# Kernel tuning notes

Hardware: AMD Instinct MI355X
Metric: run time of the kernel (lower is better)

Reference implementation:

```python
import jax, jax.numpy as jnp
import numpy as np

N = 2048            # matrix dimension (d_model-sized orthogonal factor)
BATCH = 8192        # number of row-vectors multiplied by the matrix exponential
SIGN = 1            # slogdet sign; 1 means no row negation
TRANSPOSE = False
N_FLAT = N * (N - 1) // 2


def setup_inputs() -> dict:
    key = jax.random.key(0)
    k1, k2 = jax.random.split(key)
    X = jax.random.normal(k1, (BATCH, N), dtype=jnp.float32)
    # small scale keeps the 9-term Taylor series well inside its convergence regime
    S_flat = jax.random.normal(k2, (N_FLAT,), dtype=jnp.float32) * 0.01
    return {"X": X, "S_flat": S_flat}


def _weight(S_flat):
    # unfold: scatter strict upper triangle, antisymmetrize
    rows, cols = jnp.triu_indices(N, k=1)
    M = jnp.zeros((N, N), dtype=S_flat.dtype).at[rows, cols].set(S_flat)
    S = M - M.T
    # truncated Taylor series exp(S) = I + S + S^2/2! + ... + S^9/9!
    T = S
    Q = jnp.eye(N, dtype=S.dtype) + S
    for i in range(2, 10):
        T = (T @ S) / i
        Q = Q + T
    if SIGN == -1:
        if TRANSPOSE:
            Q = Q.at[:, 0].multiply(-1.0)
        else:
            Q = Q.at[0].multiply(-1.0)
    return Q


def reference(X, S_flat):
    return X @ _weight(S_flat)
```

## Files before the change

kernel.cpp:

```cpp
#include <hip/hip_runtime.h>
#include <hip/hip_bf16.h>
#include <stdint.h>

#define N_DIM 2048
#define BATCH_SZ 8192

typedef __bf16 bf16;
typedef __bf16 bf16x4 __attribute__((ext_vector_type(4)));
typedef __bf16 bf16x8 __attribute__((ext_vector_type(8)));
typedef float f32x4 __attribute__((ext_vector_type(4)));

__device__ __forceinline__ void gld16(const bf16* g, bf16* l) {
  __builtin_amdgcn_global_load_lds(
      (const __attribute__((address_space(1))) void*)g,
      (__attribute__((address_space(3))) void*)l, 16, 0, 0);
}

__global__ void unfold_kernel(const float* __restrict__ Sflat,
                              bf16* __restrict__ Wb,
                              bf16* __restrict__ Wtb) {
  int idx = blockIdx.x * blockDim.x + threadIdx.x;
  int i = idx >> 11;
  int j = idx & (N_DIM - 1);
  float v = 0.0f;
  if (i < j) {
    int fi = i * (N_DIM - 1) - ((i * (i - 1)) >> 1) + (j - i - 1);
    v = Sflat[fi];
  } else if (i > j) {
    int fi = j * (N_DIM - 1) - ((j * (j - 1)) >> 1) + (i - j - 1);
    v = -Sflat[fi];
  }
  Wb[idx]  = (bf16)(-v);
  Wtb[idx] = (bf16)(v);
}

__global__ void cast_kernel(const float* __restrict__ in, bf16* __restrict__ out) {
  int t = blockIdx.x * blockDim.x + threadIdx.x;
  float4 v = ((const float4*)in)[t];
  bf16x4 o;
  o.x = (bf16)v.x; o.y = (bf16)v.y; o.z = (bf16)v.z; o.w = (bf16)v.w;
  ((bf16x4*)out)[t] = o;
}

template <int MODE>
__global__ __launch_bounds__(256, 2) void gemm_w(
    const bf16* __restrict__ A, const bf16* __restrict__ Bt,
    bf16* __restrict__ O1, bf16* __restrict__ O2,
    const bf16* __restrict__ Wb, int M, int N, int K) {
  __shared__ __align__(16) bf16 As[3 * 2 * 64 * 32];
  __shared__ __align__(16) bf16 Bs[3 * 2 * 128 * 32];

  const int tid  = threadIdx.x;
  const int lane = tid & 63;
  const int wave = tid >> 6;
  const int wr   = wave >> 1;
  const int wc   = wave & 1;
  const int quad = lane >> 4;
  const int l16  = lane & 15;

  const int nwg    = gridDim.x * gridDim.y;
  const int linear = blockIdx.y * gridDim.x + blockIdx.x;
  const int wg = (linear & 7) * (nwg >> 3) + (linear >> 3);
  const int bx = wg & 15;
  const int by = wg >> 4;
  const int m0 = by * 64;
  const int n0 = bx * 128;

  const int srow  = lane >> 2;
  const int sslot = (lane & 3) ^ ((lane >> 3) & 3);
  const bf16* gA  = A  + (size_t)(m0 + wave * 16 + srow) * K + sslot * 8;
  const bf16* gB1 = Bt + (size_t)(n0 + wave * 16 + srow) * K + sslot * 8;
  const bf16* gB2 = gB1 + (size_t)64 * K;
  bf16* lA  = As + wave * 512;
  bf16* lB1 = Bs + wave * 512;
  bf16* lB2 = Bs + wave * 512 + 2048;

  const int NS = K >> 6;

  auto STAGE = [&](int t, int s) {
#pragma unroll
    for (int k = 0; k < 2; ++k) {
      const size_t ko = (size_t)t * 64 + k * 32;
      gld16(gA  + ko, lA  + (s * 2 + k) * 2048);
      gld16(gB1 + ko, lB1 + (s * 2 + k) * 4096);
      gld16(gB2 + ko, lB2 + (s * 2 + k) * 4096);
    }
  };

  STAGE(0, 0);
  STAGE(1, 1);
  asm volatile("s_waitcnt vmcnt(6)" ::: "memory");
  __builtin_amdgcn_sched_barrier(0);
  __builtin_amdgcn_s_barrier();
  __builtin_amdgcn_sched_barrier(0);

  f32x4 acc[2][4] = {};
  const int rswz = (quad ^ ((l16 >> 1) & 3)) * 8;
  const int arow = wr * 32 + l16;
  const int brow = wc * 64 + l16;

  auto body = [&](int t, int s) {
    if (t + 2 < NS) STAGE(t + 2, (s + 2) % 3);
    bf16x8 af[2][2], bfr[2][4];
#pragma unroll
    for (int k = 0; k < 2; ++k) {
      const bf16* ab = As + (s * 2 + k) * 2048;
      const bf16* bb = Bs + (s * 2 + k) * 4096;
#pragma unroll
      for (int mi = 0; mi < 2; ++mi)
        af[k][mi] = *(const bf16x8*)&ab[(arow + mi * 16) * 32 + rswz];
#pragma unroll
      for (int ni = 0; ni < 4; ++ni)
        bfr[k][ni] = *(const bf16x8*)&bb[(brow + ni * 16) * 32 + rswz];
    }
    __builtin_amdgcn_s_setprio(1);
#pragma unroll
    for (int k = 0; k < 2; ++k)
#pragma unroll
      for (int mi = 0; mi < 2; ++mi)
#pragma unroll
        for (int ni = 0; ni < 4; ++ni)
          acc[mi][ni] = __builtin_amdgcn_mfma_f32_16x16x32_bf16(
              af[k][mi], bfr[k][ni], acc[mi][ni], 0, 0, 0);
    __builtin_amdgcn_s_setprio(0);
    if (t < NS - 1) {
      if (t + 2 < NS)
        asm volatile("s_waitcnt vmcnt(6)" ::: "memory");
      else
        asm volatile("s_waitcnt vmcnt(0)" ::: "memory");
      __builtin_amdgcn_sched_barrier(0);
      __builtin_amdgcn_s_barrier();
      __builtin_amdgcn_sched_barrier(0);
    }
  };

  const int NS3 = NS - (NS % 3);
#pragma unroll 1
  for (int t0 = 0; t0 < NS3; t0 += 3) {
    body(t0, 0);
    body(t0 + 1, 1);
    body(t0 + 2, 2);
  }
#pragma unroll
  for (int u = 0; u < 3; ++u) {
    const int t = NS3 + u;
    if (t < NS) body(t, u);
  }

#pragma unroll
  for (int mi = 0; mi < 2; ++mi) {
    const int r0 = m0 + wr * 32 + mi * 16 + quad * 4;
#pragma unroll
    for (int ni = 0; ni < 4; ++ni) {
      const int col = n0 + wc * 64 + ni * 16 + l16;
#pragma unroll
      for (int r = 0; r < 4; ++r) {
        const int row = r0 + r;
        const size_t idx = (size_t)row * N + col;
        const float v = acc[mi][ni][r];
        if (MODE == 1) {
          O1[idx] = (bf16)v;
          const float w = (float)Wb[idx];
          const float d = (row == col) ? 1.0f : 0.0f;
          O2[idx] = (bf16)(0.5f * d - (1.0f / 6.0f) * w + (1.0f / 24.0f) * v);
        } else {
          const float w = (float)Wb[idx];
          const float d = (row == col) ? 1.0f : 0.0f;
          O1[idx] = (bf16)(v + d + w);
        }
      }
    }
  }
}

__global__ __launch_bounds__(512, 2) void gemm256(
    const bf16* __restrict__ A, const bf16* __restrict__ Bt,
    float* __restrict__ Cf, int M, int N, int K) {
  __shared__ __align__(16) bf16 As[4 * 256 * 32];
  __shared__ __align__(16) bf16 Bs[4 * 256 * 32];

  const int tid  = threadIdx.x;
  const int lane = tid & 63;
  const int wave = tid >> 6;
  const int wr   = wave >> 2;
  const int wc   = wave & 3;
  const int quad = lane >> 4;
  const int l16  = lane & 15;

  const int nwg    = gridDim.x * gridDim.y;
  const int linear = blockIdx.y * gridDim.x + blockIdx.x;
  const int wg = (linear & 7) * (nwg >> 3) + (linear >> 3);
  const int bx = wg & 7;
  const int by = wg >> 3;
  const int m0 = by * 256;
  const int n0 = bx * 256;

  const int srow  = lane >> 2;
  const int sslot = (lane & 3) ^ ((lane >> 3) & 3);
  const bf16* pA1 = A  + (size_t)(m0 + wave * 16 + srow) * K + sslot * 8;
  const bf16* pA2 = pA1 + (size_t)128 * K;
  const bf16* pB1 = Bt + (size_t)(n0 + wave * 16 + srow) * K + sslot * 8;
  const bf16* pB2 = pB1 + (size_t)128 * K;
  bf16* lA1 = As + wave * 512;
  bf16* lA2 = As + wave * 512 + 4096;
  bf16* lB1 = Bs + wave * 512;
  bf16* lB2 = Bs + wave * 512 + 4096;

  const int NT = K >> 5;

#pragma unroll
  for (int tt = 0; tt < 3; ++tt) {
    gld16(pA1 + tt * 32, lA1 + tt * 8192);
    gld16(pA2 + tt * 32, lA2 + tt * 8192);
    gld16(pB1 + tt * 32, lB1 + tt * 8192);
    gld16(pB2 + tt * 32, lB2 + tt * 8192);
  }
  asm volatile("s_waitcnt vmcnt(8)" ::: "memory");
  __builtin_amdgcn_s_barrier();
  __builtin_amdgcn_sched_barrier(0);

  f32x4 acc[8][4] = {};
  const int rswz = (quad ^ ((l16 >> 1) & 3)) * 8;
  const int arow = wr * 128 + l16;
  const int brow = wc * 64 + l16;

  size_t kpre = 96;

#pragma unroll 1
  for (int t4 = 0; t4 < NT; t4 += 4) {
#pragma unroll
    for (int u = 0; u < 4; ++u) {
      const int t = t4 + u;
      if (t + 3 < NT) {
        const int b = (u + 3) & 3;
        const size_t ko = kpre + (size_t)u * 32;
        gld16(pA1 + ko, lA1 + b * 8192);
        gld16(pA2 + ko, lA2 + b * 8192);
        gld16(pB1 + ko, lB1 + b * 8192);
        gld16(pB2 + ko, lB2 + b * 8192);
      }
      const bf16* ab = As + u * 8192;
      const bf16* bb = Bs + u * 8192;
      bf16x8 af[8], bfr[4];
#pragma unroll
      for (int mi = 0; mi < 8; ++mi)
        af[mi] = *(const bf16x8*)&ab[(arow + mi * 16) * 32 + rswz];
#pragma unroll
      for (int ni = 0; ni < 4; ++ni)
        bfr[ni] = *(const bf16x8*)&bb[(brow + ni * 16) * 32 + rswz];
      __builtin_amdgcn_s_setprio(1);
#pragma unroll
      for (int mi = 0; mi < 8; ++mi)
#pragma unroll
        for (int ni = 0; ni < 4; ++ni)
          acc[mi][ni] = __builtin_amdgcn_mfma_f32_16x16x32_bf16(
              af[mi], bfr[ni], acc[mi][ni], 0, 0, 0);
      __builtin_amdgcn_s_setprio(0);
      if (t < NT - 1) {
        if (t < NT - 3)
          asm volatile("s_waitcnt vmcnt(8)" ::: "memory");
        else if (t == NT - 3)
          asm volatile("s_waitcnt vmcnt(4)" ::: "memory");
        else
          asm volatile("s_waitcnt vmcnt(0)" ::: "memory");
        __builtin_amdgcn_sched_barrier(0);
        __builtin_amdgcn_s_barrier();
        __builtin_amdgcn_sched_barrier(0);
      }
    }
    kpre += 128;
  }

#pragma unroll
  for (int mi = 0; mi < 8; ++mi) {
    const int r0 = m0 + wr * 128 + mi * 16 + quad * 4;
#pragma unroll
    for (int ni = 0; ni < 4; ++ni) {
      const int col = n0 + wc * 64 + ni * 16 + l16;
#pragma unroll
      for (int r = 0; r < 4; ++r)
        Cf[(size_t)(r0 + r) * N + col] = acc[mi][ni][r];
    }
  }
}

extern "C" void kernel_launch(void* const* d_in, const int* in_sizes, int n_in,
                              void* d_out, int out_size, void* d_ws, size_t ws_size,
                              hipStream_t stream) {
  const float* X     = (const float*)d_in[0];
  const float* Sflat = (const float*)d_in[1];
  float* out = (float*)d_out;
  char* ws = (char*)d_ws;

  bf16* Xb   = (bf16*)(ws);
  bf16* Wb   = (bf16*)(ws + (32u << 20));
  bf16* Wtb  = (bf16*)(ws + (40u << 20));
  bf16* W2b  = (bf16*)(ws + (48u << 20));
  bf16* Btm  = (bf16*)(ws + (56u << 20));
  bf16* Qtb  = (bf16*)(ws + (64u << 20));

  unfold_kernel<<<(N_DIM * N_DIM) / 256, 256, 0, stream>>>(Sflat, Wb, Wtb);
  cast_kernel<<<(BATCH_SZ * N_DIM / 4) / 256, 256, 0, stream>>>(X, Xb);

  const dim3 gW(N_DIM / 128, N_DIM / 64);
  gemm_w<1><<<gW, 256, 0, stream>>>(Wb, Wtb, W2b, Btm, Wb,
                                    N_DIM, N_DIM, N_DIM);
  gemm_w<2><<<gW, 256, 0, stream>>>(W2b, Btm, Qtb, nullptr, Wb,
                                    N_DIM, N_DIM, N_DIM);
  gemm256<<<dim3(N_DIM / 256, BATCH_SZ / 256), 512, 0, stream>>>(
      Xb, Qtb, out, BATCH_SZ, N_DIM, N_DIM);
}
```

Measured before the change: 263.1 us.

## Shrink weight-GEMM tiles to 64x64 and fold the X cast into the first GEMM

The two 2048^3 weight GEMMs move from 64x128 tiles with a 3-stage, 64-wide K pipeline to 64x64 tiles with a 4-stage, 32-wide K pipeline. This gives 1024 workgroups instead of 256, raises launch bounds to 5 blocks per CU, and uses less LDS, so more of the 256 CUs stay busy. The separate X float-to-bf16 cast kernel is removed; its work now runs in 256 extra workgroups of the first GEMM's grid, which saves a launch and overlaps the memory-bound cast with compute. The cost is lower per-tile data reuse, with more global and LDS traffic per FLOP, and more barriers per K.

```diff
diff --git a/kernel.cpp b/kernel.cpp
--- a/kernel.cpp
+++ b/kernel.cpp
@@ -34,21 +34,30 @@
   Wtb[idx] = (bf16)(v);
 }
 
-__global__ void cast_kernel(const float* __restrict__ in, bf16* __restrict__ out) {
-  int t = blockIdx.x * blockDim.x + threadIdx.x;
-  float4 v = ((const float4*)in)[t];
-  bf16x4 o;
-  o.x = (bf16)v.x; o.y = (bf16)v.y; o.z = (bf16)v.z; o.w = (bf16)v.w;
-  ((bf16x4*)out)[t] = o;
-}
-
-template <int MODE>
-__global__ __launch_bounds__(256, 2) void gemm_w(
+template <int MODE, int CAST>
+__global__ __launch_bounds__(256, 5) void gemm_w64(
     const bf16* __restrict__ A, const bf16* __restrict__ Bt,
     bf16* __restrict__ O1, bf16* __restrict__ O2,
-    const bf16* __restrict__ Wb, int M, int N, int K) {
-  __shared__ __align__(16) bf16 As[3 * 2 * 64 * 32];
-  __shared__ __align__(16) bf16 Bs[3 * 2 * 128 * 32];
+    const bf16* __restrict__ Wb,
+    const float* __restrict__ Xsrc, bf16* __restrict__ Xdst,
+    int M, int N, int K) {
+  __shared__ __align__(16) bf16 As[4 * 64 * 32];
+  __shared__ __align__(16) bf16 Bs[4 * 64 * 32];
+
+  if (CAST && blockIdx.y >= 32) {
+    const int id = (blockIdx.y - 32) * 32 + blockIdx.x;
+    const float4* src = (const float4*)Xsrc;
+    bf16x4* dst = (bf16x4*)Xdst;
+    const int base = id * 16384;
+#pragma unroll 4
+    for (int k = 0; k < 64; ++k) {
+      float4 v = src[base + k * 256 + threadIdx.x];
+      bf16x4 o;
+      o.x = (bf16)v.x; o.y = (bf16)v.y; o.z = (bf16)v.z; o.w = (bf16)v.w;
+      dst[base + k * 256 + threadIdx.x] = o;
+    }
+    return;
+  }
 
   const int tid  = threadIdx.x;
   const int lane = tid & 63;
@@ -58,101 +67,85 @@
   const int quad = lane >> 4;
   const int l16  = lane & 15;
 
-  const int nwg    = gridDim.x * gridDim.y;
-  const int linear = blockIdx.y * gridDim.x + blockIdx.x;
+  const int nwg    = 1024;
+  const int linear = blockIdx.y * 32 + blockIdx.x;
   const int wg = (linear & 7) * (nwg >> 3) + (linear >> 3);
-  const int bx = wg & 15;
-  const int by = wg >> 4;
+  const int bx = wg & 31;
+  const int by = wg >> 5;
   const int m0 = by * 64;
-  const int n0 = bx * 128;
+  const int n0 = bx * 64;
 
   const int srow  = lane >> 2;
   const int sslot = (lane & 3) ^ ((lane >> 3) & 3);
-  const bf16* gA  = A  + (size_t)(m0 + wave * 16 + srow) * K + sslot * 8;
-  const bf16* gB1 = Bt + (size_t)(n0 + wave * 16 + srow) * K + sslot * 8;
-  const bf16* gB2 = gB1 + (size_t)64 * K;
-  bf16* lA  = As + wave * 512;
-  bf16* lB1 = Bs + wave * 512;
-  bf16* lB2 = Bs + wave * 512 + 2048;
-
-  const int NS = K >> 6;
-
-  auto STAGE = [&](int t, int s) {
-#pragma unroll
-    for (int k = 0; k < 2; ++k) {
-      const size_t ko = (size_t)t * 64 + k * 32;
-      gld16(gA  + ko, lA  + (s * 2 + k) * 2048);
-      gld16(gB1 + ko, lB1 + (s * 2 + k) * 4096);
-      gld16(gB2 + ko, lB2 + (s * 2 + k) * 4096);
-    }
-  };
-
-  STAGE(0, 0);
-  STAGE(1, 1);
-  asm volatile("s_waitcnt vmcnt(6)" ::: "memory");
+  const bf16* gA = A  + (size_t)(m0 + wave * 16 + srow) * K + sslot * 8;
+  const bf16* gB = Bt + (size_t)(n0 + wave * 16 + srow) * K + sslot * 8;
+  bf16* lA = As + wave * 512;
+  bf16* lB = Bs + wave * 512;
+
+  const int NT = K >> 5;
+
+#pragma unroll
+  for (int tt = 0; tt < 3; ++tt) {
+    gld16(gA + tt * 32, lA + tt * 2048);
+    gld16(gB + tt * 32, lB + tt * 2048);
+  }
+  asm volatile("s_waitcnt vmcnt(4)" ::: "memory");
   __builtin_amdgcn_sched_barrier(0);
   __builtin_amdgcn_s_barrier();
   __builtin_amdgcn_sched_barrier(0);
 
-  f32x4 acc[2][4] = {};
+  f32x4 acc[2][2] = {};
   const int rswz = (quad ^ ((l16 >> 1) & 3)) * 8;
   const int arow = wr * 32 + l16;
-  const int brow = wc * 64 + l16;
-
-  auto body = [&](int t, int s) {
-    if (t + 2 < NS) STAGE(t + 2, (s + 2) % 3);
-    bf16x8 af[2][2], bfr[2][4];
-#pragma unroll
-    for (int k = 0; k < 2; ++k) {
-      const bf16* ab = As + (s * 2 + k) * 2048;
-      const bf16* bb = Bs + (s * 2 + k) * 4096;
+  const int brow = wc * 32 + l16;
+
+#pragma unroll 1
+  for (int t4 = 0; t4 < NT; t4 += 4) {
+#pragma unroll
+    for (int u = 0; u < 4; ++u) {
+      const int t = t4 + u;
+      if (t + 3 < NT) {
+        const int b = (u + 3) & 3;
+        gld16(gA + (size_t)(t + 3) * 32, lA + b * 2048);
+        gld16(gB + (size_t)(t + 3) * 32, lB + b * 2048);
+      }
+      const bf16* ab = As + u * 2048;
+      const bf16* bb = Bs + u * 2048;
+      bf16x8 af[2], bfr[2];
 #pragma unroll
       for (int mi = 0; mi < 2; ++mi)
-        af[k][mi] = *(const bf16x8*)&ab[(arow + mi * 16) * 32 + rswz];
-#pragma unroll
-      for (int ni = 0; ni < 4; ++ni)
-        bfr[k][ni] = *(const bf16x8*)&bb[(brow + ni * 16) * 32 + rswz];
-    }
-    __builtin_amdgcn_s_setprio(1);
-#pragma unroll
-    for (int k = 0; k < 2; ++k)
+        af[mi] = *(const bf16x8*)&ab[(arow + mi * 16) * 32 + rswz];
+#pragma unroll
+      for (int ni = 0; ni < 2; ++ni)
+        bfr[ni] = *(const bf16x8*)&bb[(brow + ni * 16) * 32 + rswz];
+      __builtin_amdgcn_s_setprio(1);
 #pragma unroll
       for (int mi = 0; mi < 2; ++mi)
 #pragma unroll
-        for (int ni = 0; ni < 4; ++ni)
+        for (int ni = 0; ni < 2; ++ni)
           acc[mi][ni] = __builtin_amdgcn_mfma_f32_16x16x32_bf16(
-              af[k][mi], bfr[k][ni], acc[mi][ni], 0, 0, 0);
-    __builtin_amdgcn_s_setprio(0);
-    if (t < NS - 1) {
-      if (t + 2 < NS)
-        asm volatile("s_waitcnt vmcnt(6)" ::: "memory");
-      else
-        asm volatile("s_waitcnt vmcnt(0)" ::: "memory");
-      __builtin_amdgcn_sched_barrier(0);
-      __builtin_amdgcn_s_barrier();
-      __builtin_amdgcn_sched_barrier(0);
-    }
-  };
-
-  const int NS3 = NS - (NS % 3);
-#pragma unroll 1
-  for (int t0 = 0; t0 < NS3; t0 += 3) {
-    body(t0, 0);
-    body(t0 + 1, 1);
-    body(t0 + 2, 2);
-  }
-#pragma unroll
-  for (int u = 0; u < 3; ++u) {
-    const int t = NS3 + u;
-    if (t < NS) body(t, u);
+              af[mi], bfr[ni], acc[mi][ni], 0, 0, 0);
+      __builtin_amdgcn_s_setprio(0);
+      if (t < NT - 1) {
+        if (t < NT - 3)
+          asm volatile("s_waitcnt vmcnt(4)" ::: "memory");
+        else if (t == NT - 3)
+          asm volatile("s_waitcnt vmcnt(2)" ::: "memory");
+        else
+          asm volatile("s_waitcnt vmcnt(0)" ::: "memory");
+        __builtin_amdgcn_sched_barrier(0);
+        __builtin_amdgcn_s_barrier();
+        __builtin_amdgcn_sched_barrier(0);
+      }
+    }
   }
 
 #pragma unroll
   for (int mi = 0; mi < 2; ++mi) {
     const int r0 = m0 + wr * 32 + mi * 16 + quad * 4;
 #pragma unroll
-    for (int ni = 0; ni < 4; ++ni) {
-      const int col = n0 + wc * 64 + ni * 16 + l16;
+    for (int ni = 0; ni < 2; ++ni) {
+      const int col = n0 + wc * 32 + ni * 16 + l16;
 #pragma unroll
       for (int r = 0; r < 4; ++r) {
         const int row = r0 + r;
@@ -300,13 +293,11 @@
   bf16* Qtb  = (bf16*)(ws + (64u << 20));
 
   unfold_kernel<<<(N_DIM * N_DIM) / 256, 256, 0, stream>>>(Sflat, Wb, Wtb);
-  cast_kernel<<<(BATCH_SZ * N_DIM / 4) / 256, 256, 0, stream>>>(X, Xb);
-
-  const dim3 gW(N_DIM / 128, N_DIM / 64);
-  gemm_w<1><<<gW, 256, 0, stream>>>(Wb, Wtb, W2b, Btm, Wb,
-                                    N_DIM, N_DIM, N_DIM);
-  gemm_w<2><<<gW, 256, 0, stream>>>(W2b, Btm, Qtb, nullptr, Wb,
-                                    N_DIM, N_DIM, N_DIM);
+
+  gemm_w64<1, 1><<<dim3(32, 40), 256, 0, stream>>>(
+      Wb, Wtb, W2b, Btm, Wb, X, Xb, N_DIM, N_DIM, N_DIM);
+  gemm_w64<2, 0><<<dim3(32, 32), 256, 0, stream>>>(
+      W2b, Btm, Qtb, nullptr, Wb, nullptr, nullptr, N_DIM, N_DIM, N_DIM);
   gemm256<<<dim3(N_DIM / 256, BATCH_SZ / 256), 512, 0, stream>>>(
       Xb, Qtb, out, BATCH_SZ, N_DIM, N_DIM);
 }
```

After: 277.9 us. 1.06x slower.
